# Kernel optimization log

Hardware: AMD Instinct MI355X
Metric: run time of the kernel (lower is better)

Reference implementation:

```python
import jax, jax.numpy as jnp
import numpy as np

EMBED, HID, H = 1024, 1024, 16
D = HID // H
B, L = 4, 4096


def setup_inputs() -> dict:
    key = jax.random.key(0)
    ks = jax.random.split(key, 16)
    s = 0.02
    return {
        "emb": jax.random.normal(ks[0], (B, L, EMBED), jnp.float32),
        "Wa_w": jax.random.normal(ks[1], (HID, EMBED), jnp.float32) * s,
        "Wa_b": jnp.zeros((HID,), jnp.float32),
        "Wb_w": jax.random.normal(ks[2], (HID, EMBED), jnp.float32) * s,
        "Wb_b": jnp.zeros((HID,), jnp.float32),
        "Wo_w": jax.random.normal(ks[3], (HID, EMBED), jnp.float32) * s,
        "Wo_b": jnp.zeros((HID,), jnp.float32),
        "C_w": jax.random.normal(ks[4], (HID, HID), jnp.float32) * s,
        "C_b": jnp.zeros((HID,), jnp.float32),
        "ln_g": jnp.ones((HID,), jnp.float32),
        "ln_b": jnp.zeros((HID,), jnp.float32),
        "f1_w": jax.random.normal(ks[5], (4 * HID, HID), jnp.float32) * s,
        "f1_b": jnp.zeros((4 * HID,), jnp.float32),
        "f2_w": jax.random.normal(ks[6], (HID, 4 * HID), jnp.float32) * s,
        "f2_b": jnp.zeros((HID,), jnp.float32),
        "p_w": jax.random.normal(ks[7], (HID, HID), jnp.float32) * s,
        "p_b": jnp.zeros((HID,), jnp.float32),
        "head_weights": jnp.ones((H,), jnp.float32),
    }


def _layernorm(x, g, b, eps=1e-5):
    mu = jnp.mean(x, axis=-1, keepdims=True)
    var = jnp.mean(jnp.square(x - mu), axis=-1, keepdims=True)
    return (x - mu) * jax.lax.rsqrt(var + eps) * g + b


def _affine_combine(x, y):
    a1, b1 = x
    a2, b2 = y
    return a1 * a2, a2 * b1 + b2


def reference(emb, Wa_w, Wa_b, Wb_w, Wb_b, Wo_w, Wo_b, C_w, C_b, ln_g, ln_b,
              f1_w, f1_b, f2_w, f2_b, p_w, p_b, head_weights):
    Bv, Lv, _ = emb.shape
    a = jnp.tanh(emb @ Wa_w.T + Wa_b).reshape(Bv, Lv, H, D)
    b = (emb @ Wb_w.T + Wb_b).reshape(Bv, Lv, H, D)
    w = (emb @ Wo_w.T + Wo_b).reshape(Bv, Lv, H, D)
    # h_t = a_t * h_{t-1} + b_t, h_0 = 0 -> parallel associative scan over L
    _, h_seq = jax.lax.associative_scan(_affine_combine, (a, b), axis=1)
    # batched per-step C projection over full hidden dim
    c_out = (h_seq.reshape(Bv, Lv, HID) @ C_w.T + C_b).reshape(Bv, Lv, H, D)
    z = (head_weights[None, None, :, None] * (c_out + w)).reshape(Bv, Lv, HID)
    u = z + _layernorm(z, ln_g, ln_b)
    ffn = jax.nn.gelu(u @ f1_w.T + f1_b, approximate=False)
    out = ffn @ f2_w.T + f2_b
    return (u + out) @ p_w.T + p_b
```

## Files before the change

### kernel.cpp

```cpp
#include <hip/hip_runtime.h>
#include <hip/hip_bf16.h>

typedef __attribute__((ext_vector_type(8))) short short8;
typedef __attribute__((ext_vector_type(4))) float f32x4;

#define DEVI static __device__ __forceinline__

constexpr int HID = 1024;
constexpr int BB = 4, LL = 4096;
constexpr int MROWS = BB * LL;
constexpr int NCH = 64, TCH = 64;

constexpr size_t ELN_EMB  = 0;
constexpr size_t ELN_WABO = 16777216;
constexpr size_t ELN_CW   = 19922944;
constexpr size_t ELN_F1   = 20971520;
constexpr size_t ELN_F2   = 25165824;
constexpr size_t ELN_PW   = 29360128;
constexpr size_t ELN_END  = 30408704;
constexpr size_t POOL_BYTES = ELN_END * 2;

constexpr size_t OFF_ABW = POOL_BYTES;
constexpr size_t OFF_H   = OFF_ABW + (size_t)MROWS*3072*2;
constexpr size_t OFF_U   = OFF_H  + (size_t)MROWS*1024*2;
constexpr size_t OFF_AGG = OFF_U  + (size_t)MROWS*1024*2;
constexpr size_t AG_ELEMS = (size_t)BB * NCH * HID;
constexpr size_t WS_NEEDED = OFF_AGG + AG_ELEMS * 4 * 3;

DEVI unsigned short f2b(float x) {
  unsigned u = __float_as_uint(x);
  return (unsigned short)((u + 0x7fffu + ((u >> 16) & 1u)) >> 16);
}
DEVI float b2f(unsigned short u) { return __uint_as_float((unsigned)u << 16); }

DEVI float fast_tanh(float y) {
  y = fminf(fmaxf(y, -10.f), 10.f);
  float e = __expf(2.f * y);
  return (e - 1.f) / (e + 1.f);
}
DEVI float gelu_fast(float x) {
  float t = 0.7978845608028654f * (x + 0.044715f * x * x * x);
  return 0.5f * x * (1.f + fast_tanh(t));
}

DEVI void gload_lds16(const unsigned short* g, unsigned short* l) {
  __builtin_amdgcn_global_load_lds(
      (const __attribute__((address_space(1))) void*)g,
      (__attribute__((address_space(3))) void*)l, 16, 0, 0);
}
DEVI void sbar() { __builtin_amdgcn_s_barrier(); }

constexpr long CH_EMB = 16777216 / 8;
constexpr long CH_W   = 1048576 / 8;
constexpr long CH_F   = 4194304 / 8;
constexpr long SEG1 = CH_EMB;
constexpr long SEG2 = SEG1 + CH_W;
constexpr long SEG3 = SEG2 + CH_W;
constexpr long SEG4 = SEG3 + CH_W;
constexpr long SEG5 = SEG4 + CH_W;
constexpr long SEG6 = SEG5 + CH_F;
constexpr long SEG7 = SEG6 + CH_F;
constexpr long SEG8 = SEG7 + CH_W;

__global__ __launch_bounds__(256) void convert_all(
    const float* __restrict__ emb, const float* __restrict__ wa,
    const float* __restrict__ wb,  const float* __restrict__ wo,
    const float* __restrict__ cw,  const float* __restrict__ f1,
    const float* __restrict__ f2,  const float* __restrict__ pw,
    unsigned short* __restrict__ dst) {
  const long stride = (long)gridDim.x * blockDim.x;
  for (long ck = (long)blockIdx.x * blockDim.x + threadIdx.x; ck < SEG8; ck += stride) {
    const float* s; size_t d;
    if (ck < SEG1)      { s = emb + (size_t)ck * 8;        d = ELN_EMB + (size_t)ck * 8; }
    else if (ck < SEG2) { s = wa + (size_t)(ck-SEG1) * 8;  d = ELN_WABO + (size_t)(ck-SEG1) * 8; }
    else if (ck < SEG3) { s = wb + (size_t)(ck-SEG2) * 8;  d = ELN_WABO + 1048576 + (size_t)(ck-SEG2) * 8; }
    else if (ck < SEG4) { s = wo + (size_t)(ck-SEG3) * 8;  d = ELN_WABO + 2097152 + (size_t)(ck-SEG3) * 8; }
    else if (ck < SEG5) { s = cw + (size_t)(ck-SEG4) * 8;  d = ELN_CW + (size_t)(ck-SEG4) * 8; }
    else if (ck < SEG6) { s = f1 + (size_t)(ck-SEG5) * 8;  d = ELN_F1 + (size_t)(ck-SEG5) * 8; }
    else if (ck < SEG7) { s = f2 + (size_t)(ck-SEG6) * 8;  d = ELN_F2 + (size_t)(ck-SEG6) * 8; }
    else                { s = pw + (size_t)(ck-SEG7) * 8;  d = ELN_PW + (size_t)(ck-SEG7) * 8; }
    float4 x = *(const float4*)s;
    float4 y = *(const float4*)(s + 4);
    short8 o;
    o[0]=(short)f2b(x.x); o[1]=(short)f2b(x.y); o[2]=(short)f2b(x.z); o[3]=(short)f2b(x.w);
    o[4]=(short)f2b(y.x); o[5]=(short)f2b(y.y); o[6]=(short)f2b(y.z); o[7]=(short)f2b(y.w);
    *(short8*)(dst + d) = o;
  }
}

template <int EPI>
__global__ __launch_bounds__(512) void gemm256(
    const unsigned short* __restrict__ A, const unsigned short* __restrict__ Bw,
    int K, int NITER, int ldo, int addld,
    const float* __restrict__ biasA, const float* __restrict__ biasB,
    const float* __restrict__ biasW,
    const unsigned short* __restrict__ addB, const float* __restrict__ hw,
    float* __restrict__ outF, unsigned short* __restrict__ outB) {
  __shared__ alignas(16) unsigned short lds[2][2][16384];
  const int tid = threadIdx.x;
  const int lane = tid & 63, wave = tid >> 6;
  const int wr = wave >> 2, wc = wave & 3;
  const int arow0 = blockIdx.x * 256, bcol0 = blockIdx.y * 256;
  f32x4 acc[8][4] = {};
  const int fm = lane & 15, fg = lane >> 4;
  const int sA = (fg ^ (fm & 7)) * 8;
  const int sB = ((4 + fg) ^ (fm & 7)) * 8;
  const int NT = NITER * 2;

#define MKSRC(l)                                                                   \
  const unsigned short* src##l; {                                                  \
    const int row_ = (tid >> 3) + 64 * l;                                          \
    const int c_ = (tid & 7) ^ (row_ & 7);                                         \
    src##l = (c_ < 4) ? A + (size_t)(arow0 + row_) * K + c_ * 8                    \
                      : Bw + (size_t)(bcol0 + row_) * K + (c_ - 4) * 8; }
  MKSRC(0) MKSRC(1) MKSRC(2) MKSRC(3)
#undef MKSRC

#define STG0(bf, ks, kt) do { const int ko_ = (kt) * 64 + (ks) * 32;               \
    gload_lds16(src0 + ko_, &lds[bf][ks][tid * 8]);                                \
    gload_lds16(src1 + ko_, &lds[bf][ks][4096 + tid * 8]); } while (0)
#define STG1(bf, ks, kt) do { const int ko_ = (kt) * 64 + (ks) * 32;               \
    gload_lds16(src2 + ko_, &lds[bf][ks][8192 + tid * 8]);                         \
    gload_lds16(src3 + ko_, &lds[bf][ks][12288 + tid * 8]); } while (0)

  short8 bfr[4];
#define PHASE(BUF, KS, MH, NEWB, STG, DOVM) do {                                   \
    const unsigned short* lab = &lds[BUF][KS][0];                                  \
    if (NEWB) {                                                                    \
      _Pragma("unroll") for (int n = 0; n < 4; ++n)                                \
        bfr[n] = *(const short8*)(lab + (wc * 64 + n * 16 + fm) * 64 + sB);        \
    }                                                                              \
    short8 af[4];                                                                  \
    _Pragma("unroll") for (int m = 0; m < 4; ++m)                                  \
      af[m] = *(const short8*)(lab + (wr * 128 + MH * 64 + m * 16 + fm) * 64 + sA);\
    STG;                                                                           \
    __builtin_amdgcn_s_setprio(1);                                                 \
    _Pragma("unroll") for (int m = 0; m < 4; ++m)                                  \
      _Pragma("unroll") for (int n = 0; n < 4; ++n)                                \
        acc[MH * 4 + m][n] = __builtin_amdgcn_mfma_f32_16x16x32_bf16(              \
            af[m], bfr[n], acc[MH * 4 + m][n], 0, 0, 0);                           \
    __builtin_amdgcn_s_setprio(0);                                                 \
    if (DOVM) asm volatile("s_waitcnt vmcnt(8)" ::: "memory");                     \
    sbar();                                                                        \
    __builtin_amdgcn_sched_barrier(0);                                             \
  } while (0)

  STG0(0, 0, 0); STG1(0, 0, 0);
  STG0(0, 1, 0); STG1(0, 1, 0);
  STG0(1, 0, 1); STG1(1, 0, 1);
  asm volatile("s_waitcnt vmcnt(8)" ::: "memory");
  sbar();
  __builtin_amdgcn_sched_barrier(0);

  for (int it = 0; it < NITER; ++it) {
    const int t1 = 2 * it + 1;
    const int t2 = (2 * it + 2 < NT) ? 2 * it + 2 : 0;
    const int t3 = (2 * it + 3 < NT) ? 2 * it + 3 : 1;
    PHASE(0, 0, 0, true,  STG0(1, 1, t1), false);
    PHASE(0, 0, 1, false, STG1(1, 1, t1), true);
    PHASE(0, 1, 0, true,  STG0(0, 0, t2), false);
    PHASE(0, 1, 1, false, STG1(0, 0, t2), true);
    PHASE(1, 0, 0, true,  STG0(0, 1, t2), false);
    PHASE(1, 0, 1, false, STG1(0, 1, t2), true);
    PHASE(1, 1, 0, true,  STG0(1, 0, t3), false);
    PHASE(1, 1, 1, false, STG1(1, 0, t3), true);
  }
#undef PHASE
#undef STG0
#undef STG1

  const int crow = (lane >> 4) * 4, ccol = lane & 15;
#pragma unroll
  for (int m = 0; m < 8; ++m) {
    const int row0 = arow0 + wr * 128 + (m >> 2) * 64 + (m & 3) * 16 + crow;
#pragma unroll
    for (int n = 0; n < 4; ++n) {
      const int col = bcol0 + wc * 64 + n * 16 + ccol;
#pragma unroll
      for (int r = 0; r < 4; ++r) {
        const size_t orow = (size_t)(row0 + r);
        float x = acc[m][n][r];
        if constexpr (EPI == 0) {
          const int cb = col >> 10;
          const float* bp = (cb == 0) ? biasA : (cb == 1 ? biasB : biasW);
          x += bp[col & 1023];
          if (cb == 0) x = fast_tanh(x);
          outB[orow * 3072 + col] = f2b(x);
        } else if constexpr (EPI == 1) {
          x += biasA[col] + b2f(addB[orow * (size_t)addld + col]);
          x *= hw[col >> 6];
          outB[orow * (size_t)ldo + col] = f2b(x);
        } else if constexpr (EPI == 2) {
          x += biasA[col];
          outB[orow * (size_t)ldo + col] = f2b(gelu_fast(x));
        } else if constexpr (EPI == 3) {
          x += biasA[col] + b2f(addB[orow * (size_t)addld + col]);
          outB[orow * (size_t)ldo + col] = f2b(x);
        } else {
          outF[orow * (size_t)ldo + col] = x + biasA[col];
        }
      }
    }
  }
}

__global__ __launch_bounds__(256) void scan_p1(const unsigned short* __restrict__ abw,
                                               float* __restrict__ agA,
                                               float* __restrict__ agB) {
  const int idx = blockIdx.x;
  const int cg = idx & 3, ch = (idx >> 2) & (NCH - 1), bb = idx >> 8;
  const int c = cg * 256 + threadIdx.x;
  const size_t base = ((size_t)bb * LL + (size_t)ch * TCH) * 3072 + c;
  float A = 1.f, Bg = 0.f;
#pragma unroll 4
  for (int t = 0; t < TCH; ++t) {
    float at = b2f(abw[base + (size_t)t * 3072]);
    float bt = b2f(abw[base + (size_t)t * 3072 + 1024]);
    Bg = fmaf(at, Bg, bt);
    A *= at;
  }
  const size_t o = ((size_t)bb * NCH + ch) * HID + c;
  agA[o] = A;
  agB[o] = Bg;
}

__global__ __launch_bounds__(256) void scan_p2(const float* __restrict__ agA,
                                               const float* __restrict__ agB,
                                               float* __restrict__ pre) {
  const int gid = blockIdx.x * 256 + threadIdx.x;
  const int bb = gid >> 10, c = gid & 1023;
  float h = 0.f;
  for (int ch = 0; ch < NCH; ++ch) {
    const size_t o = ((size_t)bb * NCH + ch) * HID + c;
    pre[o] = h;
    h = fmaf(agA[o], h, agB[o]);
  }
}

__global__ __launch_bounds__(256) void scan_p3(const unsigned short* __restrict__ abw,
                                               const float* __restrict__ pre,
                                               unsigned short* __restrict__ hout) {
  const int idx = blockIdx.x;
  const int cg = idx & 3, ch = (idx >> 2) & (NCH - 1), bb = idx >> 8;
  const int c = cg * 256 + threadIdx.x;
  const size_t base = ((size_t)bb * LL + (size_t)ch * TCH) * 3072 + c;
  const size_t hbase = ((size_t)bb * LL + (size_t)ch * TCH) * HID + c;
  float h = pre[((size_t)bb * NCH + ch) * HID + c];
#pragma unroll 4
  for (int t = 0; t < TCH; ++t) {
    float at = b2f(abw[base + (size_t)t * 3072]);
    float bt = b2f(abw[base + (size_t)t * 3072 + 1024]);
    h = fmaf(at, h, bt);
    hout[hbase + (size_t)t * HID] = f2b(h);
  }
}

__global__ __launch_bounds__(256) void ln_kernel(const unsigned short* __restrict__ abw,
                                                 const float* __restrict__ gam,
                                                 const float* __restrict__ bet,
                                                 unsigned short* __restrict__ u) {
  const int wave = threadIdx.x >> 6, lane = threadIdx.x & 63;
  const int row = blockIdx.x * 4 + wave;
  const unsigned short* zr = abw + (size_t)row * 3072 + lane * 16;
  short8 z0 = *(const short8*)zr;
  short8 z1 = *(const short8*)(zr + 8);
  float x[16];
#pragma unroll
  for (int e = 0; e < 8; ++e) {
    x[e]     = b2f((unsigned short)z0[e]);
    x[8 + e] = b2f((unsigned short)z1[e]);
  }
  float s = 0.f, s2 = 0.f;
#pragma unroll
  for (int e = 0; e < 16; ++e) { s += x[e]; s2 += x[e] * x[e]; }
#pragma unroll
  for (int off = 32; off > 0; off >>= 1) {
    s += __shfl_xor(s, off, 64);
    s2 += __shfl_xor(s2, off, 64);
  }
  const float mu = s * (1.f / 1024.f);
  const float var = s2 * (1.f / 1024.f) - mu * mu;
  const float rs = rsqrtf(var + 1e-5f);
  const float* gp = gam + lane * 16;
  const float* bp = bet + lane * 16;
  short8 o0, o1;
#pragma unroll
  for (int e = 0; e < 8; ++e) {
    float v0 = x[e]     + (x[e]     - mu) * rs * gp[e]     + bp[e];
    float v1 = x[8 + e] + (x[8 + e] - mu) * rs * gp[8 + e] + bp[8 + e];
    o0[e] = (short)f2b(v0);
    o1[e] = (short)f2b(v1);
  }
  unsigned short* ur = u + (size_t)row * HID + lane * 16;
  *(short8*)ur = o0;
  *(short8*)(ur + 8) = o1;
}

extern "C" void kernel_launch(void* const* d_in, const int* in_sizes, int n_in,
                              void* d_out, int out_size, void* d_ws, size_t ws_size,
                              hipStream_t stream) {
  if (ws_size < WS_NEEDED) return;

  const float* emb   = (const float*)d_in[0];
  const float* Wa_w  = (const float*)d_in[1];
  const float* Wa_b  = (const float*)d_in[2];
  const float* Wb_w  = (const float*)d_in[3];
  const float* Wb_b  = (const float*)d_in[4];
  const float* Wo_w  = (const float*)d_in[5];
  const float* Wo_b  = (const float*)d_in[6];
  const float* C_w   = (const float*)d_in[7];
  const float* C_b   = (const float*)d_in[8];
  const float* ln_g  = (const float*)d_in[9];
  const float* ln_b  = (const float*)d_in[10];
  const float* f1_w  = (const float*)d_in[11];
  const float* f1_b  = (const float*)d_in[12];
  const float* f2_w  = (const float*)d_in[13];
  const float* f2_b  = (const float*)d_in[14];
  const float* p_w   = (const float*)d_in[15];
  const float* p_b   = (const float*)d_in[16];
  const float* headw = (const float*)d_in[17];

  char* ws = (char*)d_ws;
  unsigned short* bfp  = (unsigned short*)ws;
  unsigned short* abwB = (unsigned short*)(ws + OFF_ABW);
  unsigned short* hB   = (unsigned short*)(ws + OFF_H);
  unsigned short* uB   = (unsigned short*)(ws + OFF_U);
  unsigned short* ffnB = abwB;
  float* agA = (float*)(ws + OFF_AGG);
  float* agB = agA + AG_ELEMS;
  float* pre = agB + AG_ELEMS;

  convert_all<<<2048, 256, 0, stream>>>(emb, Wa_w, Wb_w, Wo_w, C_w, f1_w, f2_w, p_w, bfp);

  gemm256<0><<<dim3(64, 12), 512, 0, stream>>>(
      bfp + ELN_EMB, bfp + ELN_WABO, 1024, 8, 3072, 0,
      Wa_b, Wb_b, Wo_b, nullptr, nullptr, nullptr, abwB);

  scan_p1<<<BB * NCH * 4, 256, 0, stream>>>(abwB, agA, agB);
  scan_p2<<<16, 256, 0, stream>>>(agA, agB, pre);
  scan_p3<<<BB * NCH * 4, 256, 0, stream>>>(abwB, pre, hB);

  gemm256<1><<<dim3(64, 4), 512, 0, stream>>>(
      hB, bfp + ELN_CW, 1024, 8, 3072, 3072,
      C_b, nullptr, nullptr, abwB + 2048, headw, nullptr, abwB);

  ln_kernel<<<4096, 256, 0, stream>>>(abwB, ln_g, ln_b, uB);

  gemm256<2><<<dim3(64, 16), 512, 0, stream>>>(
      uB, bfp + ELN_F1, 1024, 8, 4096, 0,
      f1_b, nullptr, nullptr, nullptr, nullptr, nullptr, ffnB);

  gemm256<3><<<dim3(64, 4), 512, 0, stream>>>(
      ffnB, bfp + ELN_F2, 4096, 32, 1024, 1024,
      f2_b, nullptr, nullptr, uB, nullptr, nullptr, uB);

  gemm256<4><<<dim3(64, 4), 512, 0, stream>>>(
      uB, bfp + ELN_PW, 1024, 8, 1024, 0,
      p_b, nullptr, nullptr, nullptr, nullptr, (float*)d_out, nullptr);
}
```

Measured before the change: 563.0 us.

## Switch GEMM inner loop to 32x32x16 bf16 MFMA tiles

```diff
diff --git a/kernel.cpp b/kernel.cpp
--- a/kernel.cpp
+++ b/kernel.cpp
@@ -3,6 +3,7 @@
 
 typedef __attribute__((ext_vector_type(8))) short short8;
 typedef __attribute__((ext_vector_type(4))) float f32x4;
+typedef __attribute__((ext_vector_type(16))) float f32x16;
 
 #define DEVI static __device__ __forceinline__
 
@@ -101,10 +102,8 @@
   const int lane = tid & 63, wave = tid >> 6;
   const int wr = wave >> 2, wc = wave & 3;
   const int arow0 = blockIdx.x * 256, bcol0 = blockIdx.y * 256;
-  f32x4 acc[8][4] = {};
-  const int fm = lane & 15, fg = lane >> 4;
-  const int sA = (fg ^ (fm & 7)) * 8;
-  const int sB = ((4 + fg) ^ (fm & 7)) * 8;
+  f32x16 acc[4][2] = {};
+  const int l31 = lane & 31, fg = lane >> 5, l7 = lane & 7;
   const int NT = NITER * 2;
 
 #define MKSRC(l)                                                                   \
@@ -123,24 +122,25 @@
     gload_lds16(src2 + ko_, &lds[bf][ks][8192 + tid * 8]);                         \
     gload_lds16(src3 + ko_, &lds[bf][ks][12288 + tid * 8]); } while (0)
 
-  short8 bfr[4];
-#define PHASE(BUF, KS, MH, NEWB, STG, DOVM) do {                                   \
+#define PHASE(BUF, KS, STGA, STGB) do {                                            \
     const unsigned short* lab = &lds[BUF][KS][0];                                  \
-    if (NEWB) {                                                                    \
-      _Pragma("unroll") for (int n = 0; n < 4; ++n)                                \
-        bfr[n] = *(const short8*)(lab + (wc * 64 + n * 16 + fm) * 64 + sB);        \
+    _Pragma("unroll") for (int ki = 0; ki < 2; ++ki) {                             \
+      short8 af[4], bfr[2];                                                        \
+      const int sA = ((2 * ki + fg) ^ l7) * 8;                                     \
+      const int sB = ((4 + 2 * ki + fg) ^ l7) * 8;                                 \
+      _Pragma("unroll") for (int nt = 0; nt < 2; ++nt)                             \
+        bfr[nt] = *(const short8*)(lab + (wc * 64 + nt * 32 + l31) * 64 + sB);     \
+      _Pragma("unroll") for (int mt = 0; mt < 4; ++mt)                             \
+        af[mt] = *(const short8*)(lab + (wr * 128 + mt * 32 + l31) * 64 + sA);     \
+      if (ki == 0) { STGA; } else { STGB; }                                        \
+      __builtin_amdgcn_s_setprio(1);                                               \
+      _Pragma("unroll") for (int mt = 0; mt < 4; ++mt)                             \
+        _Pragma("unroll") for (int nt = 0; nt < 2; ++nt)                           \
+          acc[mt][nt] = __builtin_amdgcn_mfma_f32_32x32x16_bf16(                   \
+              af[mt], bfr[nt], acc[mt][nt], 0, 0, 0);                              \
+      __builtin_amdgcn_s_setprio(0);                                               \
     }                                                                              \
-    short8 af[4];                                                                  \
-    _Pragma("unroll") for (int m = 0; m < 4; ++m)                                  \
-      af[m] = *(const short8*)(lab + (wr * 128 + MH * 64 + m * 16 + fm) * 64 + sA);\
-    STG;                                                                           \
-    __builtin_amdgcn_s_setprio(1);                                                 \
-    _Pragma("unroll") for (int m = 0; m < 4; ++m)                                  \
-      _Pragma("unroll") for (int n = 0; n < 4; ++n)                                \
-        acc[MH * 4 + m][n] = __builtin_amdgcn_mfma_f32_16x16x32_bf16(              \
-            af[m], bfr[n], acc[MH * 4 + m][n], 0, 0, 0);                           \
-    __builtin_amdgcn_s_setprio(0);                                                 \
-    if (DOVM) asm volatile("s_waitcnt vmcnt(8)" ::: "memory");                     \
+    asm volatile("s_waitcnt vmcnt(8)" ::: "memory");                               \
     sbar();                                                                        \
     __builtin_amdgcn_sched_barrier(0);                                             \
   } while (0)
@@ -156,48 +156,49 @@
     const int t1 = 2 * it + 1;
     const int t2 = (2 * it + 2 < NT) ? 2 * it + 2 : 0;
     const int t3 = (2 * it + 3 < NT) ? 2 * it + 3 : 1;
-    PHASE(0, 0, 0, true,  STG0(1, 1, t1), false);
-    PHASE(0, 0, 1, false, STG1(1, 1, t1), true);
-    PHASE(0, 1, 0, true,  STG0(0, 0, t2), false);
-    PHASE(0, 1, 1, false, STG1(0, 0, t2), true);
-    PHASE(1, 0, 0, true,  STG0(0, 1, t2), false);
-    PHASE(1, 0, 1, false, STG1(0, 1, t2), true);
-    PHASE(1, 1, 0, true,  STG0(1, 0, t3), false);
-    PHASE(1, 1, 1, false, STG1(1, 0, t3), true);
+    PHASE(0, 0, STG0(1, 1, t1), STG1(1, 1, t1));
+    PHASE(0, 1, STG0(0, 0, t2), STG1(0, 0, t2));
+    PHASE(1, 0, STG0(0, 1, t2), STG1(0, 1, t2));
+    PHASE(1, 1, STG0(1, 0, t3), STG1(1, 0, t3));
   }
 #undef PHASE
 #undef STG0
 #undef STG1
 
-  const int crow = (lane >> 4) * 4, ccol = lane & 15;
-#pragma unroll
-  for (int m = 0; m < 8; ++m) {
-    const int row0 = arow0 + wr * 128 + (m >> 2) * 64 + (m & 3) * 16 + crow;
-#pragma unroll
-    for (int n = 0; n < 4; ++n) {
-      const int col = bcol0 + wc * 64 + n * 16 + ccol;
-#pragma unroll
-      for (int r = 0; r < 4; ++r) {
-        const size_t orow = (size_t)(row0 + r);
-        float x = acc[m][n][r];
+  const int rb = 4 * fg;
+#pragma unroll
+  for (int mt = 0; mt < 4; ++mt) {
+#pragma unroll
+    for (int nt = 0; nt < 2; ++nt) {
+      const int col = bcol0 + wc * 64 + nt * 32 + l31;
+      const int row0 = arow0 + wr * 128 + mt * 32 + rb;
+      float bv;
+      float hwv = 1.f;
+      if constexpr (EPI == 0) {
+        const int cb = col >> 10;
+        bv = ((cb == 0) ? biasA : (cb == 1 ? biasB : biasW))[col & 1023];
+      } else {
+        bv = biasA[col];
+        if constexpr (EPI == 1) hwv = hw[col >> 6];
+      }
+#pragma unroll
+      for (int g = 0; g < 16; ++g) {
+        const int row = row0 + (g & 3) + 8 * (g >> 2);
+        const size_t orow = (size_t)row;
+        float x = acc[mt][nt][g] + bv;
         if constexpr (EPI == 0) {
-          const int cb = col >> 10;
-          const float* bp = (cb == 0) ? biasA : (cb == 1 ? biasB : biasW);
-          x += bp[col & 1023];
-          if (cb == 0) x = fast_tanh(x);
+          if ((col >> 10) == 0) x = fast_tanh(x);
           outB[orow * 3072 + col] = f2b(x);
         } else if constexpr (EPI == 1) {
-          x += biasA[col] + b2f(addB[orow * (size_t)addld + col]);
-          x *= hw[col >> 6];
+          x = hwv * (x + b2f(addB[orow * (size_t)addld + col]));
           outB[orow * (size_t)ldo + col] = f2b(x);
         } else if constexpr (EPI == 2) {
-          x += biasA[col];
           outB[orow * (size_t)ldo + col] = f2b(gelu_fast(x));
         } else if constexpr (EPI == 3) {
-          x += biasA[col] + b2f(addB[orow * (size_t)addld + col]);
+          x += b2f(addB[orow * (size_t)addld + col]);
           outB[orow * (size_t)ldo + col] = f2b(x);
         } else {
-          outF[orow * (size_t)ldo + col] = x + biasA[col];
+          outF[orow * (size_t)ldo + col] = x;
         }
       }
     }
```

After: 598.4 us. +6.3%, slower.
